# Performance work log

Measured on AMD Instinct MI355X. Metric: run time of the kernel, lower is better.

## Reference

```python
import jax, jax.numpy as jnp
import numpy as np

FIELDS = 32
EMBED = 64
PAIRS = FIELDS * (FIELDS - 1) // 2  # 496
BATCH = 2048


def setup_inputs() -> dict:
    key = jax.random.key(0)
    k1, k2 = jax.random.split(key)
    x = jax.random.normal(k1, (BATCH, FIELDS, EMBED), dtype=jnp.float32)
    kernel = jax.random.normal(k2, (EMBED, PAIRS, EMBED), dtype=jnp.float32) * 0.05
    return {"x": x, "kernel": kernel}


def reference(x, kernel):
    # Pair enumeration (i<j) matching the python double loop order.
    iu, ju = jnp.triu_indices(FIELDS, k=1)
    p = x[:, iu, :]  # (B, P, E)
    q = x[:, ju, :]  # (B, P, E)
    # Original: kp[b,f,pr] = sum_e p[b,pr,e]*kernel[f,pr,e];
    # result[b,pr] = sum_f kp[b,f,pr]*q[b,pr,f]
    # => bilinear form per pair, fused as a single einsum.
    result = jnp.einsum('bpe,fpe,bpf->bp', p, kernel, q)
    return result
```

## Files before the change

kernel.cpp:

```cpp
#include <hip/hip_runtime.h>
#include <hip/hip_bf16.h>


constexpr int BATCH  = 2048;
constexpr int FIELDS = 32;
constexpr int EMBED  = 64;
constexpr int PAIRS  = FIELDS * (FIELDS - 1) / 2;

typedef __attribute__((ext_vector_type(8))) short  short8;
typedef __attribute__((ext_vector_type(4))) float  f32x4;

constexpr size_t XN      = (size_t)BATCH * FIELDS * EMBED;
constexpr size_t KPN     = (size_t)PAIRS * 2 * 4 * 64 * 8;
constexpr size_t XH_OFF  = 0;
constexpr size_t XL_OFF  = XH_OFF + XN * 2;
constexpr size_t KPH_OFF = XL_OFF + XN * 2;
constexpr size_t KPL_OFF = KPH_OFF + KPN * 2;
constexpr size_t WS_NEED = KPL_OFF + KPN * 2;

__device__ __forceinline__ unsigned short f32_to_bf16_rne(float f) {
    unsigned int u = __float_as_uint(f);
    u = u + 0x7fffu + ((u >> 16) & 1u);
    return (unsigned short)(u >> 16);
}
__device__ __forceinline__ float bf16_bits_to_f32(unsigned short h) {
    return __uint_as_float(((unsigned int)h) << 16);
}

__global__ __launch_bounds__(256) void convert_x_kernel(
    const float* __restrict__ x,
    unsigned short* __restrict__ xh,
    unsigned short* __restrict__ xl)
{
    const int idx = (int)blockIdx.x * 256 + (int)threadIdx.x;
    const float4 v = ((const float4*)x)[idx];
    const float vv[4] = {v.x, v.y, v.z, v.w};
    unsigned short h[4], l[4];
    #pragma unroll
    for (int j = 0; j < 4; ++j) {
        const unsigned short hb = f32_to_bf16_rne(vv[j]);
        h[j] = hb;
        l[j] = f32_to_bf16_rne(vv[j] - bf16_bits_to_f32(hb));
    }
    ((ushort4*)xh)[idx] = make_ushort4(h[0], h[1], h[2], h[3]);
    ((ushort4*)xl)[idx] = make_ushort4(l[0], l[1], l[2], l[3]);
}

__global__ __launch_bounds__(256) void pack_k_kernel(
    const float* __restrict__ kern,
    unsigned short* __restrict__ kph,
    unsigned short* __restrict__ kpl)
{
    const int t    = (int)blockIdx.x * 256 + (int)threadIdx.x;
    const int lane = t & 63;
    const int nc   = (t >> 6) & 3;
    const int ks   = (t >> 8) & 1;
    const int pair = t >> 9;
    const int e    = nc * 16 + (lane & 15);
    const int f0   = ks * 32 + (lane >> 4) * 8;

    unsigned short h[8], l[8];
    #pragma unroll
    for (int jj = 0; jj < 8; ++jj) {
        const float v = kern[((size_t)(f0 + jj) * PAIRS + pair) * EMBED + e];
        const unsigned short hb = f32_to_bf16_rne(v);
        h[jj] = hb;
        l[jj] = f32_to_bf16_rne(v - bf16_bits_to_f32(hb));
    }
    #pragma unroll
    for (int jj = 0; jj < 8; ++jj) {
        kph[(size_t)t * 8 + jj] = h[jj];
        kpl[(size_t)t * 8 + jj] = l[jj];
    }
}

__global__ __launch_bounds__(256) void opn_mfma_kernel(
    const float* __restrict__ x,
    const unsigned short* __restrict__ xh,
    const unsigned short* __restrict__ xl,
    const unsigned short* __restrict__ kph,
    const unsigned short* __restrict__ kpl,
    float* __restrict__ out)
{
    const int bid  = (int)blockIdx.x;
    const int p    = bid >> 3;
    const int mt   = bid & 7;
    const int wave = (int)threadIdx.x >> 6;
    const int lane = (int)threadIdx.x & 63;
    const int Mb   = mt * 256 + wave * 64;
    const int g    = lane >> 4;
    const int c    = lane & 15;

    int i = 0, rem = p;
    while (rem >= FIELDS - 1 - i) { rem -= FIELDS - 1 - i; ++i; }
    const int jf = i + 1 + rem;

    f32x4 acc[4][4];
    #pragma unroll
    for (int mr = 0; mr < 4; ++mr)
        #pragma unroll
        for (int nc = 0; nc < 4; ++nc)
            acc[mr][nc] = (f32x4){0.f, 0.f, 0.f, 0.f};

    #pragma unroll
    for (int ks = 0; ks < 2; ++ks) {
        short8 ah[4], al[4];
        #pragma unroll
        for (int mr = 0; mr < 4; ++mr) {
            const int row = Mb + mr * 16 + c;
            const size_t off = ((size_t)row * FIELDS + jf) * EMBED + ks * 32 + g * 8;
            ah[mr] = *(const short8*)(xh + off);
            al[mr] = *(const short8*)(xl + off);
        }
        short8 bh[4], bl[4];
        #pragma unroll
        for (int nc = 0; nc < 4; ++nc) {
            const size_t kidx = (((size_t)(p * 2 + ks) * 4 + nc) * 64 + lane) * 8;
            bh[nc] = *(const short8*)(kph + kidx);
            bl[nc] = *(const short8*)(kpl + kidx);
        }
        #pragma unroll
        for (int mr = 0; mr < 4; ++mr) {
            #pragma unroll
            for (int nc = 0; nc < 4; ++nc) {
                acc[mr][nc] = __builtin_amdgcn_mfma_f32_16x16x32_bf16(ah[mr], bh[nc], acc[mr][nc], 0, 0, 0);
                acc[mr][nc] = __builtin_amdgcn_mfma_f32_16x16x32_bf16(ah[mr], bl[nc], acc[mr][nc], 0, 0, 0);
                acc[mr][nc] = __builtin_amdgcn_mfma_f32_16x16x32_bf16(al[mr], bh[nc], acc[mr][nc], 0, 0, 0);
            }
        }
    }

    float z[4][4];
    #pragma unroll
    for (int mr = 0; mr < 4; ++mr)
        #pragma unroll
        for (int t = 0; t < 4; ++t)
            z[mr][t] = 0.f;

    const size_t xi_base = (size_t)i * EMBED + c;
    #pragma unroll
    for (int mr = 0; mr < 4; ++mr) {
        #pragma unroll
        for (int t = 0; t < 4; ++t) {
            const int row = Mb + mr * 16 + 4 * g + t;
            const float* xi = x + (size_t)row * (FIELDS * EMBED) + xi_base;
            #pragma unroll
            for (int nc = 0; nc < 4; ++nc)
                z[mr][t] = fmaf(acc[mr][nc][t], xi[nc * 16], z[mr][t]);
        }
    }

    #pragma unroll
    for (int mask = 1; mask < 16; mask <<= 1) {
        #pragma unroll
        for (int mr = 0; mr < 4; ++mr)
            #pragma unroll
            for (int t = 0; t < 4; ++t)
                z[mr][t] += __shfl_xor(z[mr][t], mask, 64);
    }

    if (c < 4) {
        const int t = c;
        #pragma unroll
        for (int mr = 0; mr < 4; ++mr) {
            const int row = Mb + mr * 16 + 4 * g + t;
            out[(size_t)row * PAIRS + p] = z[mr][t];
        }
    }
}

constexpr int BT     = 64;
constexpr int BTILES = BATCH / BT;

__global__ __launch_bounds__(64) void opn_fp32_kernel(
    const float* __restrict__ x,
    const float* __restrict__ kern,
    float* __restrict__ out)
{
    const int bid   = (int)blockIdx.x;
    const int p     = bid >> 5;
    const int btile = bid & (BTILES - 1);
    const int lane  = (int)threadIdx.x;
    const int b     = btile * BT + lane;

    int i = 0, rem = p;
    while (rem >= FIELDS - 1 - i) { rem -= FIELDS - 1 - i; ++i; }
    const int j = i + 1 + rem;

    const float* xrow_i = x + (size_t)b * (FIELDS * EMBED) + i * EMBED;
    const float* xrow_j = x + (size_t)b * (FIELDS * EMBED) + j * EMBED;
    const float* kp     = kern + (size_t)p * EMBED;

    float acc[EMBED];
    #pragma unroll
    for (int e = 0; e < EMBED; ++e) acc[e] = 0.0f;

    const float4* xj4 = (const float4*)xrow_j;
    #pragma unroll 2
    for (int f4 = 0; f4 < EMBED / 4; ++f4) {
        const float4 v = xj4[f4];
        const float xjf[4] = {v.x, v.y, v.z, v.w};
        #pragma unroll
        for (int s = 0; s < 4; ++s) {
            const float* kf = kp + (size_t)(f4 * 4 + s) * (PAIRS * EMBED);
            #pragma unroll
            for (int e = 0; e < EMBED; ++e)
                acc[e] = fmaf(xjf[s], kf[e], acc[e]);
        }
    }

    float r = 0.0f;
    const float4* xi4 = (const float4*)xrow_i;
    #pragma unroll
    for (int e4 = 0; e4 < EMBED / 4; ++e4) {
        const float4 u = xi4[e4];
        r = fmaf(u.x, acc[e4 * 4 + 0], r);
        r = fmaf(u.y, acc[e4 * 4 + 1], r);
        r = fmaf(u.z, acc[e4 * 4 + 2], r);
        r = fmaf(u.w, acc[e4 * 4 + 3], r);
    }
    out[(size_t)b * PAIRS + p] = r;
}

extern "C" void kernel_launch(void* const* d_in, const int* in_sizes, int n_in,
                              void* d_out, int out_size, void* d_ws, size_t ws_size,
                              hipStream_t stream) {
    const float* x    = (const float*)d_in[0];
    const float* kern = (const float*)d_in[1];
    float*       out  = (float*)d_out;

    if (ws_size < WS_NEED) {
        opn_fp32_kernel<<<dim3(PAIRS * BTILES), dim3(64), 0, stream>>>(x, kern, out);
        return;
    }

    char* ws = (char*)d_ws;
    unsigned short* xhi = (unsigned short*)(ws + XH_OFF);
    unsigned short* xlo = (unsigned short*)(ws + XL_OFF);
    unsigned short* kph = (unsigned short*)(ws + KPH_OFF);
    unsigned short* kpl = (unsigned short*)(ws + KPL_OFF);

    convert_x_kernel<<<dim3((unsigned)(XN / 4 / 256)), dim3(256), 0, stream>>>(x, xhi, xlo);
    pack_k_kernel<<<dim3((unsigned)(PAIRS * 2 * 4 * 64 / 256)), dim3(256), 0, stream>>>(kern, kph, kpl);
    opn_mfma_kernel<<<dim3(PAIRS * 8), dim3(256), 0, stream>>>(x, xhi, xlo, kph, kpl, out);
}
```

Measured before the change: 126.5 us.

## Merge prep kernels, shrink MFMA tile, reorder grid pair-major for reuse

Fuses the x split and kernel packing into one launch, which removes a kernel launch. The high bf16 part is now a plain truncation, with the residual still rounded, and the K pack writes vectorised short8 stores. The MFMA kernel now covers 32 rows per wave instead of 64 and doubles the grid. Blocks are ordered pair-fastest so that adjacent blocks share x rows in cache, and launch bounds request occupancy 3. Truncating the high part changes how the split error is distributed but keeps hi+lo close to fp32.

```diff
diff --git a/kernel.cpp b/kernel.cpp
--- a/kernel.cpp
+++ b/kernel.cpp
@@ -1,5 +1,4 @@
 #include <hip/hip_runtime.h>
-#include <hip/hip_bf16.h>
 
 
 constexpr int BATCH  = 2048;
@@ -18,63 +17,62 @@
 constexpr size_t KPL_OFF = KPH_OFF + KPN * 2;
 constexpr size_t WS_NEED = KPL_OFF + KPN * 2;
 
-__device__ __forceinline__ unsigned short f32_to_bf16_rne(float f) {
+constexpr int XSPLIT_BLOCKS = (int)(XN / 4 / 256);
+constexpr int KPACK_BLOCKS  = (int)(PAIRS * 512 / 256);
+
+__device__ __forceinline__ unsigned short bf16_rne(float f) {
     unsigned int u = __float_as_uint(f);
     u = u + 0x7fffu + ((u >> 16) & 1u);
     return (unsigned short)(u >> 16);
 }
-__device__ __forceinline__ float bf16_bits_to_f32(unsigned short h) {
-    return __uint_as_float(((unsigned int)h) << 16);
-}
-
-__global__ __launch_bounds__(256) void convert_x_kernel(
+
+__global__ __launch_bounds__(256) void prep_kernel(
     const float* __restrict__ x,
+    const float* __restrict__ kern,
     unsigned short* __restrict__ xh,
-    unsigned short* __restrict__ xl)
-{
-    const int idx = (int)blockIdx.x * 256 + (int)threadIdx.x;
-    const float4 v = ((const float4*)x)[idx];
-    const float vv[4] = {v.x, v.y, v.z, v.w};
-    unsigned short h[4], l[4];
-    #pragma unroll
-    for (int j = 0; j < 4; ++j) {
-        const unsigned short hb = f32_to_bf16_rne(vv[j]);
-        h[j] = hb;
-        l[j] = f32_to_bf16_rne(vv[j] - bf16_bits_to_f32(hb));
-    }
-    ((ushort4*)xh)[idx] = make_ushort4(h[0], h[1], h[2], h[3]);
-    ((ushort4*)xl)[idx] = make_ushort4(l[0], l[1], l[2], l[3]);
-}
-
-__global__ __launch_bounds__(256) void pack_k_kernel(
-    const float* __restrict__ kern,
+    unsigned short* __restrict__ xl,
     unsigned short* __restrict__ kph,
     unsigned short* __restrict__ kpl)
 {
-    const int t    = (int)blockIdx.x * 256 + (int)threadIdx.x;
-    const int lane = t & 63;
-    const int nc   = (t >> 6) & 3;
-    const int ks   = (t >> 8) & 1;
-    const int pair = t >> 9;
-    const int e    = nc * 16 + (lane & 15);
-    const int f0   = ks * 32 + (lane >> 4) * 8;
-
-    unsigned short h[8], l[8];
-    #pragma unroll
-    for (int jj = 0; jj < 8; ++jj) {
-        const float v = kern[((size_t)(f0 + jj) * PAIRS + pair) * EMBED + e];
-        const unsigned short hb = f32_to_bf16_rne(v);
-        h[jj] = hb;
-        l[jj] = f32_to_bf16_rne(v - bf16_bits_to_f32(hb));
-    }
-    #pragma unroll
-    for (int jj = 0; jj < 8; ++jj) {
-        kph[(size_t)t * 8 + jj] = h[jj];
-        kpl[(size_t)t * 8 + jj] = l[jj];
-    }
-}
-
-__global__ __launch_bounds__(256) void opn_mfma_kernel(
+    const int bid = (int)blockIdx.x;
+    const int tid = (int)threadIdx.x;
+
+    if (bid < XSPLIT_BLOCKS) {
+        const int idx = bid * 256 + tid;
+        const float4 v = ((const float4*)x)[idx];
+        const float vv[4] = {v.x, v.y, v.z, v.w};
+        unsigned short h[4], l[4];
+        #pragma unroll
+        for (int j = 0; j < 4; ++j) {
+            const unsigned int u = __float_as_uint(vv[j]);
+            h[j] = (unsigned short)(u >> 16);
+            l[j] = bf16_rne(vv[j] - __uint_as_float(u & 0xffff0000u));
+        }
+        ((ushort4*)xh)[idx] = make_ushort4(h[0], h[1], h[2], h[3]);
+        ((ushort4*)xl)[idx] = make_ushort4(l[0], l[1], l[2], l[3]);
+    } else {
+        const int t    = (bid - XSPLIT_BLOCKS) * 256 + tid;
+        const int lane = t & 63;
+        const int nc   = (t >> 6) & 3;
+        const int ks   = (t >> 8) & 1;
+        const int pair = t >> 9;
+        const int e    = nc * 16 + (lane & 15);
+        const int f0   = ks * 32 + (lane >> 4) * 8;
+
+        short8 h8, l8;
+        #pragma unroll
+        for (int jj = 0; jj < 8; ++jj) {
+            const float v = kern[((size_t)(f0 + jj) * PAIRS + pair) * EMBED + e];
+            const unsigned int u = __float_as_uint(v);
+            h8[jj] = (short)(u >> 16);
+            l8[jj] = (short)bf16_rne(v - __uint_as_float(u & 0xffff0000u));
+        }
+        *(short8*)(kph + (size_t)t * 8) = h8;
+        *(short8*)(kpl + (size_t)t * 8) = l8;
+    }
+}
+
+__global__ __launch_bounds__(256, 3) void opn_mfma_kernel(
     const float* __restrict__ x,
     const unsigned short* __restrict__ xh,
     const unsigned short* __restrict__ xl,
@@ -83,11 +81,11 @@
     float* __restrict__ out)
 {
     const int bid  = (int)blockIdx.x;
-    const int p    = bid >> 3;
-    const int mt   = bid & 7;
+    const int p    = bid % PAIRS;
+    const int mt   = bid / PAIRS;
     const int wave = (int)threadIdx.x >> 6;
     const int lane = (int)threadIdx.x & 63;
-    const int Mb   = mt * 256 + wave * 64;
+    const int Mb   = mt * 128 + wave * 32;
     const int g    = lane >> 4;
     const int c    = lane & 15;
 
@@ -95,18 +93,18 @@
     while (rem >= FIELDS - 1 - i) { rem -= FIELDS - 1 - i; ++i; }
     const int jf = i + 1 + rem;
 
-    f32x4 acc[4][4];
-    #pragma unroll
-    for (int mr = 0; mr < 4; ++mr)
+    f32x4 acc[2][4];
+    #pragma unroll
+    for (int mr = 0; mr < 2; ++mr)
         #pragma unroll
         for (int nc = 0; nc < 4; ++nc)
             acc[mr][nc] = (f32x4){0.f, 0.f, 0.f, 0.f};
 
     #pragma unroll
     for (int ks = 0; ks < 2; ++ks) {
-        short8 ah[4], al[4];
-        #pragma unroll
-        for (int mr = 0; mr < 4; ++mr) {
+        short8 ah[2], al[2];
+        #pragma unroll
+        for (int mr = 0; mr < 2; ++mr) {
             const int row = Mb + mr * 16 + c;
             const size_t off = ((size_t)row * FIELDS + jf) * EMBED + ks * 32 + g * 8;
             ah[mr] = *(const short8*)(xh + off);
@@ -120,26 +118,25 @@
             bl[nc] = *(const short8*)(kpl + kidx);
         }
         #pragma unroll
-        for (int mr = 0; mr < 4; ++mr) {
+        for (int mr = 0; mr < 2; ++mr)
             #pragma unroll
             for (int nc = 0; nc < 4; ++nc) {
                 acc[mr][nc] = __builtin_amdgcn_mfma_f32_16x16x32_bf16(ah[mr], bh[nc], acc[mr][nc], 0, 0, 0);
                 acc[mr][nc] = __builtin_amdgcn_mfma_f32_16x16x32_bf16(ah[mr], bl[nc], acc[mr][nc], 0, 0, 0);
                 acc[mr][nc] = __builtin_amdgcn_mfma_f32_16x16x32_bf16(al[mr], bh[nc], acc[mr][nc], 0, 0, 0);
             }
-        }
-    }
-
-    float z[4][4];
-    #pragma unroll
-    for (int mr = 0; mr < 4; ++mr)
+    }
+
+    float z[2][4];
+    #pragma unroll
+    for (int mr = 0; mr < 2; ++mr)
         #pragma unroll
         for (int t = 0; t < 4; ++t)
             z[mr][t] = 0.f;
 
     const size_t xi_base = (size_t)i * EMBED + c;
     #pragma unroll
-    for (int mr = 0; mr < 4; ++mr) {
+    for (int mr = 0; mr < 2; ++mr)
         #pragma unroll
         for (int t = 0; t < 4; ++t) {
             const int row = Mb + mr * 16 + 4 * g + t;
@@ -148,29 +145,24 @@
             for (int nc = 0; nc < 4; ++nc)
                 z[mr][t] = fmaf(acc[mr][nc][t], xi[nc * 16], z[mr][t]);
         }
-    }
-
-    #pragma unroll
-    for (int mask = 1; mask < 16; mask <<= 1) {
-        #pragma unroll
-        for (int mr = 0; mr < 4; ++mr)
+
+    #pragma unroll
+    for (int mask = 1; mask < 16; mask <<= 1)
+        #pragma unroll
+        for (int mr = 0; mr < 2; ++mr)
             #pragma unroll
             for (int t = 0; t < 4; ++t)
                 z[mr][t] += __shfl_xor(z[mr][t], mask, 64);
-    }
 
     if (c < 4) {
         const int t = c;
         #pragma unroll
-        for (int mr = 0; mr < 4; ++mr) {
+        for (int mr = 0; mr < 2; ++mr) {
             const int row = Mb + mr * 16 + 4 * g + t;
             out[(size_t)row * PAIRS + p] = z[mr][t];
         }
     }
 }
-
-constexpr int BT     = 64;
-constexpr int BTILES = BATCH / BT;
 
 __global__ __launch_bounds__(64) void opn_fp32_kernel(
     const float* __restrict__ x,
@@ -179,9 +171,9 @@
 {
     const int bid   = (int)blockIdx.x;
     const int p     = bid >> 5;
-    const int btile = bid & (BTILES - 1);
+    const int btile = bid & 31;
     const int lane  = (int)threadIdx.x;
-    const int b     = btile * BT + lane;
+    const int b     = btile * 64 + lane;
 
     int i = 0, rem = p;
     while (rem >= FIELDS - 1 - i) { rem -= FIELDS - 1 - i; ++i; }
@@ -230,7 +222,7 @@
     float*       out  = (float*)d_out;
 
     if (ws_size < WS_NEED) {
-        opn_fp32_kernel<<<dim3(PAIRS * BTILES), dim3(64), 0, stream>>>(x, kern, out);
+        opn_fp32_kernel<<<dim3(PAIRS * 32), dim3(64), 0, stream>>>(x, kern, out);
         return;
     }
 
@@ -240,7 +232,8 @@
     unsigned short* kph = (unsigned short*)(ws + KPH_OFF);
     unsigned short* kpl = (unsigned short*)(ws + KPL_OFF);
 
-    convert_x_kernel<<<dim3((unsigned)(XN / 4 / 256)), dim3(256), 0, stream>>>(x, xhi, xlo);
-    pack_k_kernel<<<dim3((unsigned)(PAIRS * 2 * 4 * 64 / 256)), dim3(256), 0, stream>>>(kern, kph, kpl);
-    opn_mfma_kernel<<<dim3(PAIRS * 8), dim3(256), 0, stream>>>(x, xhi, xlo, kph, kpl, out);
-}
+    prep_kernel<<<dim3(XSPLIT_BLOCKS + KPACK_BLOCKS), dim3(256), 0, stream>>>(
+        x, kern, xhi, xlo, kph, kpl);
+    opn_mfma_kernel<<<dim3(PAIRS * 16), dim3(256), 0, stream>>>(
+        x, xhi, xlo, kph, kpl, out);
+}
```

Measured after the change: 132.7 us. 1.05x slower.
